# Performance work log

Hardware: AMD Instinct MI355X
Metric: run time of the kernel (lower is better)

The kernel has to match this reference:

```python
import jax, jax.numpy as jnp
import numpy as np

B, CIN, COUT, N, R = 4, 32, 64, 65536, 32
PAD = 0.1
NEG_SLOPE = 0.1


def _norm_coords(coords):
    # coords [B,3,N] in [-1,1]; map to continuous voxel space [0, R-1]
    return jnp.clip((coords / (1.0 + PAD) + 1.0) * 0.5 * (R - 1), 0.0, R - 1)


def scatter_mean(feat, coords):
    # feat [B,C,N], coords [B,3,N] -> voxel grid [B,C,R,R,R]
    b, c, n = feat.shape
    nc = _norm_coords(coords)
    idx = jnp.clip(jnp.floor(nc + 0.5), 0, R - 1).astype(jnp.int32)  # nearest voxel
    flat = (idx[:, 0] * R + idx[:, 1]) * R + idx[:, 2]               # [B,N]
    seg = (flat + jnp.arange(b, dtype=jnp.int32)[:, None] * (R ** 3)).reshape(-1)
    f = feat.transpose(0, 2, 1).reshape(b * n, c)
    sums = jax.ops.segment_sum(f, seg, num_segments=b * R ** 3)
    cnt = jax.ops.segment_sum(jnp.ones((b * n,), feat.dtype), seg, num_segments=b * R ** 3)
    mean = sums / jnp.maximum(cnt, 1.0)[:, None]
    return mean.reshape(b, R, R, R, c).transpose(0, 4, 1, 2, 3)


def trilinear_sample(grid, coords):
    # grid [B,C,R,R,R], coords [B,3,N] -> point features [B,C,N]
    b, c = grid.shape[:2]
    n = coords.shape[-1]
    nc = _norm_coords(coords)                      # [B,3,N]
    lo = jnp.floor(nc).astype(jnp.int32)
    lo = jnp.clip(lo, 0, R - 1)
    hi = jnp.minimum(lo + 1, R - 1)
    frac = nc - lo.astype(nc.dtype)                # [B,3,N]
    gflat = grid.reshape(b, c, R ** 3).transpose(0, 2, 1)  # [B, R^3, C]

    def corner(ix, iy, iz):
        fi = (ix * R + iy) * R + iz                # [B,N]
        return jnp.take_along_axis(gflat, fi[..., None], axis=1)  # [B,N,C]

    fx, fy, fz = frac[:, 0], frac[:, 1], frac[:, 2]
    x0, y0, z0 = lo[:, 0], lo[:, 1], lo[:, 2]
    x1, y1, z1 = hi[:, 0], hi[:, 1], hi[:, 2]
    w = lambda a: a[..., None]
    out = (corner(x0, y0, z0) * w((1 - fx) * (1 - fy) * (1 - fz))
           + corner(x0, y0, z1) * w((1 - fx) * (1 - fy) * fz)
           + corner(x0, y1, z0) * w((1 - fx) * fy * (1 - fz))
           + corner(x0, y1, z1) * w((1 - fx) * fy * fz)
           + corner(x1, y0, z0) * w(fx * (1 - fy) * (1 - fz))
           + corner(x1, y0, z1) * w(fx * (1 - fy) * fz)
           + corner(x1, y1, z0) * w(fx * fy * (1 - fz))
           + corner(x1, y1, z1) * w(fx * fy * fz))
    return out.transpose(0, 2, 1)                  # [B,C,N]


def conv3d(x, w, b):
    y = jax.lax.conv_general_dilated(x, w, (1, 1, 1), 'SAME',
                                     dimension_numbers=('NCDHW', 'OIDHW', 'NCDHW'))
    return y + b[None, :, None, None, None]


def leaky(x):
    return jnp.where(x >= 0, x, NEG_SLOPE * x)


def setup_inputs() -> dict:
    key = jax.random.key(0)
    ks = jax.random.split(key, 6)
    features = jax.random.normal(ks[0], (B, CIN, N), jnp.float32)
    inputs = jax.random.uniform(ks[1], (B, 3, N), jnp.float32) * 2.0 - 1.0  # coords in [-1,1]
    w_mlp = jax.random.normal(ks[2], (COUT, CIN), jnp.float32) * 0.05
    b_mlp = jnp.zeros((COUT,), jnp.float32)
    w_conv1 = jax.random.normal(ks[3], (COUT, CIN, 3, 3, 3), jnp.float32) * 0.05
    b_conv1 = jnp.zeros((COUT,), jnp.float32)
    w_conv2 = jax.random.normal(ks[4], (COUT, COUT, 3, 3, 3), jnp.float32) * 0.05
    b_conv2 = jnp.zeros((COUT,), jnp.float32)
    return {"features": features, "inputs": inputs, "w_mlp": w_mlp, "b_mlp": b_mlp,
            "w_conv1": w_conv1, "b_conv1": b_conv1, "w_conv2": w_conv2, "b_conv2": b_conv2}


def reference(features, inputs, w_mlp, b_mlp, w_conv1, b_conv1, w_conv2, b_conv2):
    # First PVConv layer: voxelize point features (scatter-mean)
    voxel_in = scatter_mean(features, inputs)                     # [B,CIN,R,R,R]
    # point branch: Conv1d(k=1) + ReLU (mlp=False path, norm=None)
    point_feature = jax.nn.relu(jnp.einsum('oc,bcn->bon', w_mlp, features) + b_mlp[None, :, None])
    # voxel branch: DoubleConv = (conv3d -> leaky_relu) x 2, layer_order 'cna' with norm=None
    v = leaky(conv3d(voxel_in, w_conv1, b_conv1))
    voxel_feature = leaky(conv3d(v, w_conv2, b_conv2))            # [B,COUT,R,R,R]
    # fuse point feature: trilinear devoxelization gather + add
    sampled = trilinear_sample(voxel_feature, inputs)             # [B,COUT,N]
    point_out = point_feature + sampled
    return (point_out, voxel_feature)
```

## Files before the change

### kernel.cpp

```cpp
#include <hip/hip_runtime.h>

typedef unsigned short ushort_t;
typedef unsigned int uint_t;
typedef __attribute__((ext_vector_type(4))) float f32x4;
typedef __attribute__((ext_vector_type(16))) float f32x16;
typedef __attribute__((ext_vector_type(4))) unsigned int u32x4;
typedef __attribute__((ext_vector_type(8))) short short8;

#define R3 32768
#define NPTS 65536

__device__ __forceinline__ float bf_lo(uint_t u) { return __uint_as_float(u << 16); }
__device__ __forceinline__ float bf_hi(uint_t u) { return __uint_as_float(u & 0xffff0000u); }
__device__ __forceinline__ ushort_t f2b(float f) {
    uint_t u = __float_as_uint(f);
    u += 0x7fffu + ((u >> 16) & 1u);
    return (ushort_t)(u >> 16);
}
__device__ __forceinline__ float normc(float c) {
    float v = (c / 1.1f + 1.0f) * 0.5f * 31.0f;
    return fminf(fmaxf(v, 0.0f), 31.0f);
}

__global__ __launch_bounds__(256) void k_vid(const float* __restrict__ coords,
                                             int* __restrict__ vid,
                                             uint_t* __restrict__ hist) {
    int gid = blockIdx.x * 256 + threadIdx.x;
    int b = gid >> 16, n = gid & 65535;
    const float* cp = coords + (size_t)b * 3 * NPTS + n;
    int ix = (int)floorf(normc(cp[0]) + 0.5f);
    int iy = (int)floorf(normc(cp[NPTS]) + 0.5f);
    int iz = (int)floorf(normc(cp[2 * NPTS]) + 0.5f);
    ix = min(max(ix, 0), 31); iy = min(max(iy, 0), 31); iz = min(max(iz, 0), 31);
    int v = b * R3 + ((ix * 32 + iy) * 32 + iz);
    vid[gid] = v;
    atomicAdd(hist + v, 1u);
}

__global__ __launch_bounds__(256) void k_scanA(const uint_t* __restrict__ hist,
                                               uint_t* __restrict__ excl,
                                               uint_t* __restrict__ bsum) {
    __shared__ uint_t sh[256];
    int t = threadIdx.x;
    int base = blockIdx.x * 1024 + t * 4;
    uint_t v0 = hist[base], v1 = hist[base + 1], v2 = hist[base + 2], v3 = hist[base + 3];
    uint_t s = v0 + v1 + v2 + v3;
    sh[t] = s;
    __syncthreads();
    uint_t x = s;
    for (int off = 1; off < 256; off <<= 1) {
        uint_t y = (t >= off) ? sh[t - off] : 0u;
        __syncthreads();
        x += y;
        sh[t] = x;
        __syncthreads();
    }
    uint_t e = x - s;
    excl[base] = e;
    excl[base + 1] = e + v0;
    excl[base + 2] = e + v0 + v1;
    excl[base + 3] = e + v0 + v1 + v2;
    if (t == 255) bsum[blockIdx.x] = x;
}

__global__ __launch_bounds__(128) void k_scanB(uint_t* __restrict__ bsum,
                                               uint_t* __restrict__ boff) {
    __shared__ uint_t sh[128];
    int t = threadIdx.x;
    uint_t s = bsum[t];
    sh[t] = s;
    __syncthreads();
    uint_t x = s;
    for (int off = 1; off < 128; off <<= 1) {
        uint_t y = (t >= off) ? sh[t - off] : 0u;
        __syncthreads();
        x += y;
        sh[t] = x;
        __syncthreads();
    }
    boff[t] = x - s;
}

__global__ __launch_bounds__(256) void k_scanC(uint_t* __restrict__ excl,
                                               const uint_t* __restrict__ boff,
                                               uint_t* __restrict__ cursor) {
    int i = blockIdx.x * 256 + threadIdx.x;
    uint_t v = excl[i] + boff[i >> 10];
    excl[i] = v;
    cursor[i] = v;
}

__global__ __launch_bounds__(256) void k_scatfeat(const float* __restrict__ feat,
                                                  const int* __restrict__ vid,
                                                  uint_t* __restrict__ cursor,
                                                  ushort_t* __restrict__ sorted) {
    int gid = blockIdx.x * 256 + threadIdx.x;
    int b = gid >> 16, n = gid & 65535;
    int v = vid[gid];
    uint_t slot = atomicAdd(cursor + v, 1u);
    const float* f = feat + (size_t)b * 32 * NPTS + n;
    ushort_t* dst = sorted + (size_t)slot * 32;
#pragma unroll
    for (int q = 0; q < 4; ++q) {
        u32x4 val;
#pragma unroll
        for (int j = 0; j < 4; ++j) {
            float a = f[(size_t)(q * 8 + j * 2) * NPTS];
            float c = f[(size_t)(q * 8 + j * 2 + 1) * NPTS];
            val[j] = (uint_t)f2b(a) | ((uint_t)f2b(c) << 16);
        }
        *(u32x4*)(dst + q * 8) = val;
    }
}

__global__ __launch_bounds__(256) void k_reduce(const ushort_t* __restrict__ sorted,
                                                const uint_t* __restrict__ start,
                                                const uint_t* __restrict__ hist,
                                                ushort_t* __restrict__ mean_cl) {
    int v = blockIdx.x * 256 + threadIdx.x;
    uint_t s = start[v], c = hist[v];
    float acc[32];
#pragma unroll
    for (int i = 0; i < 32; ++i) acc[i] = 0.0f;
    for (uint_t i = 0; i < c; ++i) {
        const u32x4* p = (const u32x4*)(sorted + (size_t)(s + i) * 32);
#pragma unroll
        for (int q = 0; q < 4; ++q) {
            u32x4 val = p[q];
#pragma unroll
            for (int j = 0; j < 4; ++j) {
                acc[q * 8 + j * 2] += bf_lo(val[j]);
                acc[q * 8 + j * 2 + 1] += bf_hi(val[j]);
            }
        }
    }
    float inv = 1.0f / fmaxf((float)c, 1.0f);
    ushort_t* dst = mean_cl + (size_t)v * 32;
#pragma unroll
    for (int q = 0; q < 4; ++q) {
        u32x4 val;
#pragma unroll
        for (int j = 0; j < 4; ++j)
            val[j] = (uint_t)f2b(acc[q * 8 + j * 2] * inv) |
                     ((uint_t)f2b(acc[q * 8 + j * 2 + 1] * inv) << 16);
        *(u32x4*)(dst + q * 8) = val;
    }
}

__global__ __launch_bounds__(256) void k_wpack(const float* __restrict__ w1,
                                               const float* __restrict__ w2,
                                               ushort_t* __restrict__ Wp1,
                                               ushort_t* __restrict__ Wp2) {
    int t = blockIdx.x * 256 + threadIdx.x;
    if (t < 55296) {
        int dz = t / 18432, r = t % 18432;
        int kb = r >> 9, o = (r >> 3) & 63, ke = r & 7;
        int k = kb * 8 + ke, ci = k & 31, n9 = k >> 5;
        Wp1[t] = f2b(w1[(o * 32 + ci) * 27 + n9 * 3 + dz]);
    } else if (t < 165888) {
        int u = t - 55296;
        int dz = u / 36864, r = u % 36864;
        int kb = r >> 9, o = (r >> 3) & 63, ke = r & 7;
        int k = kb * 8 + ke, ci = k & 63, n9 = k >> 6;
        Wp2[u] = f2b(w2[(o * 64 + ci) * 27 + n9 * 3 + dz]);
    }
}

template <int CB, bool WRITE_CF>
__global__ __launch_bounds__(256) void k_conv(const ushort_t* __restrict__ in_b16,
                                              const ushort_t* __restrict__ Wp,
                                              const float* __restrict__ bias,
                                              ushort_t* __restrict__ out_cl,
                                              float* __restrict__ out_cf) {
    constexpr int CI = CB * 8;
    constexpr int PLANE_CHUNKS = CB * 10 * 19;
    __shared__ union ShU {
        ushort_t T[2][CB][10][19][8];
        float S[64][132];
    } sh;
    int tid = threadIdx.x, bid = blockIdx.x;
    int zh = bid & 1, ys = (bid >> 1) & 3, x = (bid >> 3) & 31, b = bid >> 8;
    int y0 = ys * 8, z0 = zh * 16;

    auto stage = [&](int dx, int pb) {
        int gx = x + dx - 1;
        bool xok = (unsigned)gx < 32u;
        const ushort_t* src = in_b16 + (size_t)(b * R3 + gx * 1024) * CI;
        for (int c = tid; c < PLANE_CHUNKS; c += 256) {
            int zz = c % 19, rem = c / 19;
            int yy = rem % 10, cb = rem / 10;
            int gy = y0 + yy - 1, gz = z0 + zz - 1;
            u32x4 val = {0u, 0u, 0u, 0u};
            if (xok && (unsigned)gy < 32u && (unsigned)gz < 32u)
                val = *(const u32x4*)(src + (size_t)(gy * 32 + gz) * CI + cb * 8);
            *(u32x4*)(&sh.T[pb][cb][yy][zz][0]) = val;
        }
    };

    int lane = tid & 63, wv = tid >> 6;
    int nq = wv & 1, mq = wv >> 1;
    int l31 = lane & 31, lh = lane >> 5;
    int o = nq * 32 + l31;
    int ya0 = mq * 4 + (l31 >> 4);
    int ya1 = ya0 + 2;
    int za = l31 & 15;

    f32x16 acc0, acc1;
#pragma unroll
    for (int i = 0; i < 16; ++i) { acc0[i] = 0.0f; acc1[i] = 0.0f; }

    stage(0, 0);
    __syncthreads();
#pragma unroll
    for (int dx = 0; dx < 3; ++dx) {
        if (dx < 2) stage(dx + 1, (dx + 1) & 1);
        const ushort_t* Tp = &sh.T[dx & 1][0][0][0][0];
        const ushort_t* wpB = Wp + (size_t)o * 8;
#pragma unroll
        for (int dz = 0; dz < 3; ++dz)
#pragma unroll
            for (int dy = 0; dy < 3; ++dy)
#pragma unroll
                for (int cbp = 0; cbp < CB / 2; ++cbp) {
                    int cb = cbp * 2 + lh;
                    const ushort_t* tb = Tp + (size_t)cb * 10 * 19 * 8;
                    short8 a0 = *(const short8*)(tb + ((ya0 + dy) * 19 + za + dz) * 8);
                    short8 a1 = *(const short8*)(tb + ((ya1 + dy) * 19 + za + dz) * 8);
                    int kb = (dx * 3 + dy) * CB + cb;
                    short8 bw = *(const short8*)(wpB + (size_t)(dz * 9 * CB + kb) * 512);
                    acc0 = __builtin_amdgcn_mfma_f32_32x32x16_bf16(a0, bw, acc0, 0, 0, 0);
                    acc1 = __builtin_amdgcn_mfma_f32_32x32x16_bf16(a1, bw, acc1, 0, 0, 0);
                }
        __syncthreads();
    }

    float bia = bias[o];
#pragma unroll
    for (int i = 0; i < 2; ++i) {
        int mbase = (mq * 2 + i) * 32 + lh * 4;
#pragma unroll
        for (int rq = 0; rq < 4; ++rq) {
            f32x4 v4;
#pragma unroll
            for (int j = 0; j < 4; ++j) {
                float v = (i ? acc1[rq * 4 + j] : acc0[rq * 4 + j]) + bia;
                v4[j] = (v >= 0.0f) ? v : 0.1f * v;
            }
            *(f32x4*)(&sh.S[o][mbase + rq * 8]) = v4;
        }
    }
    __syncthreads();

    {
        int vl = tid >> 1, oh = tid & 1;
        int y = vl >> 4, z = vl & 15;
        ushort_t* dst =
            out_cl + ((size_t)(b * R3 + x * 1024 + (y0 + y) * 32 + z0 + z)) * 64 + oh * 32;
#pragma unroll
        for (int q = 0; q < 4; ++q) {
            u32x4 w;
#pragma unroll
            for (int j4 = 0; j4 < 4; ++j4) {
                int oo = oh * 32 + q * 8 + j4 * 2;
                w[j4] = (uint_t)f2b(sh.S[oo][vl]) | ((uint_t)f2b(sh.S[oo + 1][vl]) << 16);
            }
            *(u32x4*)(dst + q * 8) = w;
        }
    }
    if (WRITE_CF) {
        int oo = tid >> 2, zq = tid & 3;
        float* dp = out_cf + (size_t)(b * 64 + oo) * R3 + x * 1024 + y0 * 32 + z0 + zq * 4;
#pragma unroll
        for (int y = 0; y < 8; ++y)
            *(f32x4*)(dp + y * 32) = *(const f32x4*)(&sh.S[oo][y * 16 + zq * 4]);
    }
}

__global__ __launch_bounds__(256) void k_point(const float* __restrict__ feat,
                                               const float* __restrict__ coords,
                                               const float* __restrict__ w_mlp,
                                               const float* __restrict__ b_mlp,
                                               const ushort_t* __restrict__ vf,
                                               float* __restrict__ out) {
    __shared__ int vox_s[64][8];
    __shared__ float wgt_s[64][8];
    __shared__ float S[64][65];
    int tid = threadIdx.x;
    int b = blockIdx.x >> 10;
    int p0 = (blockIdx.x & 1023) * 64;

    {
        int p = tid & 63, cpair = tid >> 6;
        const float* cp = coords + (size_t)b * 3 * NPTS + p0 + p;
        float nx = normc(cp[0]), ny = normc(cp[NPTS]), nz = normc(cp[2 * NPTS]);
        int x0 = min(max((int)floorf(nx), 0), 31);
        int y0 = min(max((int)floorf(ny), 0), 31);
        int z0 = min(max((int)floorf(nz), 0), 31);
        float fx = nx - (float)x0, fy = ny - (float)y0, fz = nz - (float)z0;
        int x1 = min(x0 + 1, 31), y1 = min(y0 + 1, 31), z1 = min(z0 + 1, 31);
#pragma unroll
        for (int j = 0; j < 2; ++j) {
            int c = cpair * 2 + j;
            int xi = (c & 4) ? x1 : x0, yi = (c & 2) ? y1 : y0, zi = (c & 1) ? z1 : z0;
            float wc = ((c & 4) ? fx : 1.0f - fx) * ((c & 2) ? fy : 1.0f - fy) *
                       ((c & 1) ? fz : 1.0f - fz);
            vox_s[p][c] = (xi * 32 + yi) * 32 + zi;
            wgt_s[p][c] = wc;
        }
    }
    __syncthreads();

    int lane = tid & 63, wv = tid >> 6;
    {
        const ushort_t* vfb = vf + (size_t)b * R3 * 64 + lane;
        for (int t = 0; t < 16; ++t) {
            int p = wv * 16 + t;
            float s = 0.0f;
#pragma unroll
            for (int c = 0; c < 8; ++c) {
                int vox = vox_s[p][c];
                float wc = wgt_s[p][c];
                uint_t raw = (uint_t)vfb[(size_t)vox * 64];
                s = fmaf(wc, __uint_as_float(raw << 16), s);
            }
            S[p][lane] = s;
        }
    }
    __syncthreads();

    {
        int o0 = __builtin_amdgcn_readfirstlane(wv) * 16;
        const float* fb = feat + (size_t)b * 32 * NPTS + p0 + lane;
        float ft[32];
#pragma unroll
        for (int ci = 0; ci < 32; ++ci) ft[ci] = fb[(size_t)ci * NPTS];
        float* ob = out + ((size_t)b * 64 + o0) * NPTS + p0 + lane;
#pragma unroll
        for (int oi = 0; oi < 16; ++oi) {
            float m = b_mlp[o0 + oi];
            const float* wrow = w_mlp + (size_t)(o0 + oi) * 32;
#pragma unroll
            for (int ci = 0; ci < 32; ++ci) m = fmaf(wrow[ci], ft[ci], m);
            m = fmaxf(m, 0.0f);
            ob[(size_t)oi * NPTS] = m + S[lane][o0 + oi];
        }
    }
}

extern "C" void kernel_launch(void* const* d_in, const int* in_sizes, int n_in,
                              void* d_out, int out_size, void* d_ws, size_t ws_size,
                              hipStream_t stream) {
    const float* feat   = (const float*)d_in[0];
    const float* coords = (const float*)d_in[1];
    const float* w_mlp  = (const float*)d_in[2];
    const float* b_mlp  = (const float*)d_in[3];
    const float* w_c1   = (const float*)d_in[4];
    const float* b_c1   = (const float*)d_in[5];
    const float* w_c2   = (const float*)d_in[6];
    const float* b_c2   = (const float*)d_in[7];

    float* out = (float*)d_out;
    float* point_out = out;
    float* vfeat = out + 16777216;

    ushort_t* sorted  = (ushort_t*)out;
    ushort_t* mean_cl = (ushort_t*)(out + 4194304);
    ushort_t* v_cl    = (ushort_t*)(out + 6291456);
    int*      vid     = (int*)(out + 10485760);
    uint_t*   hist    = (uint_t*)(out + 10747904);
    uint_t*   excl    = (uint_t*)(out + 10878976);
    uint_t*   cursor  = (uint_t*)(out + 11010048);
    uint_t*   bsum    = (uint_t*)(out + 11141120);
    uint_t*   boff    = (uint_t*)(out + 11141248);
    ushort_t* Wp1     = (ushort_t*)(out + 11141376);
    ushort_t* Wp2     = (ushort_t*)(out + 11169024);
    ushort_t* vf_cl   = (ushort_t*)d_ws;

    hipMemsetAsync(hist, 0, 131072 * 4, stream);
    k_wpack<<<648, 256, 0, stream>>>(w_c1, w_c2, Wp1, Wp2);
    k_vid<<<1024, 256, 0, stream>>>(coords, vid, hist);
    k_scanA<<<128, 256, 0, stream>>>(hist, excl, bsum);
    k_scanB<<<1, 128, 0, stream>>>(bsum, boff);
    k_scanC<<<512, 256, 0, stream>>>(excl, boff, cursor);
    k_scatfeat<<<1024, 256, 0, stream>>>(feat, vid, cursor, sorted);
    k_reduce<<<512, 256, 0, stream>>>(sorted, excl, hist, mean_cl);
    k_conv<4, false><<<1024, 256, 0, stream>>>(mean_cl, Wp1, b_c1, v_cl, (float*)nullptr);
    k_conv<8, true><<<1024, 256, 0, stream>>>(v_cl, Wp2, b_c2, vf_cl, vfeat);
    k_point<<<4096, 256, 0, stream>>>(feat, coords, w_mlp, b_mlp, vf_cl, point_out);
}
```

Measured before the change: 181.6 us.

## Read conv3d inputs directly from global memory instead of staging halo planes in LDS

The conv kernels stop staging double-buffered halo x-planes in shared memory and instead have each wave compute one y-row of 32 z voxels against all 64 output channels, loading A fragments straight from the channel-last global tensor. Out-of-range taps are skipped with early continues and z padding is handled by zero fragments. This removes the LDS staging traffic and the per-dx barriers. In exchange, neighbouring voxels are re-read from global memory or cache up to 27 times with no explicit reuse, and the block tile shrinks to 4x32 voxels.

```diff
diff --git a/kernel.cpp b/kernel.cpp
--- a/kernel.cpp
+++ b/kernel.cpp
@@ -166,113 +166,97 @@
     }
 }
 
-template <int CB, bool WRITE_CF>
-__global__ __launch_bounds__(256) void k_conv(const ushort_t* __restrict__ in_b16,
+template <int CI, bool WRITE_CF>
+__global__ __launch_bounds__(256) void k_conv(const ushort_t* __restrict__ in_cl,
                                               const ushort_t* __restrict__ Wp,
                                               const float* __restrict__ bias,
                                               ushort_t* __restrict__ out_cl,
                                               float* __restrict__ out_cf) {
-    constexpr int CI = CB * 8;
-    constexpr int PLANE_CHUNKS = CB * 10 * 19;
-    __shared__ union ShU {
-        ushort_t T[2][CB][10][19][8];
-        float S[64][132];
-    } sh;
+    constexpr int CP = CI / 16;
+    constexpr int KB9 = CI * 9 / 8;
+    __shared__ float S[64][132];
     int tid = threadIdx.x, bid = blockIdx.x;
-    int zh = bid & 1, ys = (bid >> 1) & 3, x = (bid >> 3) & 31, b = bid >> 8;
-    int y0 = ys * 8, z0 = zh * 16;
-
-    auto stage = [&](int dx, int pb) {
+    int y4 = bid & 7, x = (bid >> 3) & 31, b = bid >> 8;
+    int lane = tid & 63, wv = tid >> 6;
+    int l31 = lane & 31, lh = lane >> 5;
+    int y = y4 * 4 + wv;
+    int z = l31;
+
+    f32x16 acc0, acc1;
+#pragma unroll
+    for (int i = 0; i < 16; ++i) { acc0[i] = 0.0f; acc1[i] = 0.0f; }
+
+    const ushort_t* inb = in_cl + (size_t)b * R3 * CI;
+#pragma unroll
+    for (int dx = 0; dx < 3; ++dx) {
         int gx = x + dx - 1;
-        bool xok = (unsigned)gx < 32u;
-        const ushort_t* src = in_b16 + (size_t)(b * R3 + gx * 1024) * CI;
-        for (int c = tid; c < PLANE_CHUNKS; c += 256) {
-            int zz = c % 19, rem = c / 19;
-            int yy = rem % 10, cb = rem / 10;
-            int gy = y0 + yy - 1, gz = z0 + zz - 1;
-            u32x4 val = {0u, 0u, 0u, 0u};
-            if (xok && (unsigned)gy < 32u && (unsigned)gz < 32u)
-                val = *(const u32x4*)(src + (size_t)(gy * 32 + gz) * CI + cb * 8);
-            *(u32x4*)(&sh.T[pb][cb][yy][zz][0]) = val;
-        }
-    };
-
-    int lane = tid & 63, wv = tid >> 6;
-    int nq = wv & 1, mq = wv >> 1;
-    int l31 = lane & 31, lh = lane >> 5;
-    int o = nq * 32 + l31;
-    int ya0 = mq * 4 + (l31 >> 4);
-    int ya1 = ya0 + 2;
-    int za = l31 & 15;
-
-    f32x16 acc0, acc1;
-#pragma unroll
-    for (int i = 0; i < 16; ++i) { acc0[i] = 0.0f; acc1[i] = 0.0f; }
-
-    stage(0, 0);
-    __syncthreads();
-#pragma unroll
-    for (int dx = 0; dx < 3; ++dx) {
-        if (dx < 2) stage(dx + 1, (dx + 1) & 1);
-        const ushort_t* Tp = &sh.T[dx & 1][0][0][0][0];
-        const ushort_t* wpB = Wp + (size_t)o * 8;
-#pragma unroll
-        for (int dz = 0; dz < 3; ++dz)
-#pragma unroll
-            for (int dy = 0; dy < 3; ++dy)
-#pragma unroll
-                for (int cbp = 0; cbp < CB / 2; ++cbp) {
-                    int cb = cbp * 2 + lh;
-                    const ushort_t* tb = Tp + (size_t)cb * 10 * 19 * 8;
-                    short8 a0 = *(const short8*)(tb + ((ya0 + dy) * 19 + za + dz) * 8);
-                    short8 a1 = *(const short8*)(tb + ((ya1 + dy) * 19 + za + dz) * 8);
-                    int kb = (dx * 3 + dy) * CB + cb;
-                    short8 bw = *(const short8*)(wpB + (size_t)(dz * 9 * CB + kb) * 512);
-                    acc0 = __builtin_amdgcn_mfma_f32_32x32x16_bf16(a0, bw, acc0, 0, 0, 0);
-                    acc1 = __builtin_amdgcn_mfma_f32_32x32x16_bf16(a1, bw, acc1, 0, 0, 0);
+        if ((unsigned)gx >= 32u) continue;
+#pragma unroll
+        for (int dy = 0; dy < 3; ++dy) {
+            int gy = y + dy - 1;
+            if ((unsigned)gy >= 32u) continue;
+            int tap = dx * 3 + dy;
+            const ushort_t* colp = inb + (size_t)((gx * 32 + gy) * 32) * CI + lh * 8;
+#pragma unroll
+            for (int dz = 0; dz < 3; ++dz) {
+                int zs = z + dz - 1;
+                bool zok = (unsigned)zs < 32u;
+                const ushort_t* arow = colp + (ptrdiff_t)zs * CI;
+                const ushort_t* wb =
+                    Wp + ((size_t)(dz * KB9 + tap * (CI / 8)) * 64) * 8 + l31 * 8;
+#pragma unroll
+                for (int cp = 0; cp < CP; ++cp) {
+                    short8 a = {0, 0, 0, 0, 0, 0, 0, 0};
+                    if (zok) a = *(const short8*)(arow + cp * 16);
+                    const ushort_t* wkb = wb + (size_t)(cp * 2 + lh) * 512;
+                    short8 w0 = *(const short8*)(wkb);
+                    short8 w1 = *(const short8*)(wkb + 256);
+                    acc0 = __builtin_amdgcn_mfma_f32_32x32x16_bf16(a, w0, acc0, 0, 0, 0);
+                    acc1 = __builtin_amdgcn_mfma_f32_32x32x16_bf16(a, w1, acc1, 0, 0, 0);
                 }
-        __syncthreads();
-    }
-
-    float bia = bias[o];
-#pragma unroll
-    for (int i = 0; i < 2; ++i) {
-        int mbase = (mq * 2 + i) * 32 + lh * 4;
-#pragma unroll
-        for (int rq = 0; rq < 4; ++rq) {
-            f32x4 v4;
-#pragma unroll
-            for (int j = 0; j < 4; ++j) {
-                float v = (i ? acc1[rq * 4 + j] : acc0[rq * 4 + j]) + bia;
-                v4[j] = (v >= 0.0f) ? v : 0.1f * v;
             }
-            *(f32x4*)(&sh.S[o][mbase + rq * 8]) = v4;
-        }
+        }
+    }
+
+    float bia0 = bias[l31], bia1 = bias[32 + l31];
+#pragma unroll
+    for (int rq = 0; rq < 4; ++rq) {
+        f32x4 v0, v1;
+#pragma unroll
+        for (int j = 0; j < 4; ++j) {
+            float a = acc0[rq * 4 + j] + bia0;
+            float c = acc1[rq * 4 + j] + bia1;
+            v0[j] = (a >= 0.0f) ? a : 0.1f * a;
+            v1[j] = (c >= 0.0f) ? c : 0.1f * c;
+        }
+        int m = wv * 32 + lh * 4 + rq * 8;
+        *(f32x4*)(&S[l31][m]) = v0;
+        *(f32x4*)(&S[32 + l31][m]) = v1;
     }
     __syncthreads();
 
     {
         int vl = tid >> 1, oh = tid & 1;
-        int y = vl >> 4, z = vl & 15;
-        ushort_t* dst =
-            out_cl + ((size_t)(b * R3 + x * 1024 + (y0 + y) * 32 + z0 + z)) * 64 + oh * 32;
+        int yy = vl >> 5, zz = vl & 31;
+        ushort_t* dst = out_cl +
+            ((size_t)(b * R3 + x * 1024 + (y4 * 4 + yy) * 32 + zz)) * 64 + oh * 32;
 #pragma unroll
         for (int q = 0; q < 4; ++q) {
             u32x4 w;
 #pragma unroll
             for (int j4 = 0; j4 < 4; ++j4) {
                 int oo = oh * 32 + q * 8 + j4 * 2;
-                w[j4] = (uint_t)f2b(sh.S[oo][vl]) | ((uint_t)f2b(sh.S[oo + 1][vl]) << 16);
+                w[j4] = (uint_t)f2b(S[oo][vl]) | ((uint_t)f2b(S[oo + 1][vl]) << 16);
             }
             *(u32x4*)(dst + q * 8) = w;
         }
     }
     if (WRITE_CF) {
-        int oo = tid >> 2, zq = tid & 3;
-        float* dp = out_cf + (size_t)(b * 64 + oo) * R3 + x * 1024 + y0 * 32 + z0 + zq * 4;
-#pragma unroll
-        for (int y = 0; y < 8; ++y)
-            *(f32x4*)(dp + y * 32) = *(const f32x4*)(&sh.S[oo][y * 16 + zq * 4]);
+        int oo = tid >> 2, ti = tid & 3;
+        float* dp = out_cf + (size_t)(b * 64 + oo) * R3 + x * 1024 + y4 * 128 + ti * 4;
+#pragma unroll
+        for (int j = 0; j < 8; ++j)
+            *(f32x4*)(dp + j * 16) = *(const f32x4*)(&S[oo][ti * 4 + j * 16]);
     }
 }
 
@@ -384,7 +368,7 @@
     k_scanC<<<512, 256, 0, stream>>>(excl, boff, cursor);
     k_scatfeat<<<1024, 256, 0, stream>>>(feat, vid, cursor, sorted);
     k_reduce<<<512, 256, 0, stream>>>(sorted, excl, hist, mean_cl);
-    k_conv<4, false><<<1024, 256, 0, stream>>>(mean_cl, Wp1, b_c1, v_cl, (float*)nullptr);
-    k_conv<8, true><<<1024, 256, 0, stream>>>(v_cl, Wp2, b_c2, vf_cl, vfeat);
+    k_conv<32, false><<<1024, 256, 0, stream>>>(mean_cl, Wp1, b_c1, v_cl, (float*)nullptr);
+    k_conv<64, true><<<1024, 256, 0, stream>>>(v_cl, Wp2, b_c2, vf_cl, vfeat);
     k_point<<<4096, 256, 0, stream>>>(feat, coords, w_mlp, b_mlp, vf_cl, point_out);
 }
```

Result: slower. 217.1 us (+19.6%).
